# Performance work log

Hardware: AMD Instinct MI355X
Metric: run time of the kernel (lower is better)

Reference implementation:

```python
import jax, jax.numpy as jnp
import numpy as np

B, C, N, K = 4, 192, 8192, 16
C_OUT = 192


def _gather_nodes(xs, idx):
    # xs: [B, C, N], idx: [B, N, K] -> [B, C, N, K]
    return jax.vmap(lambda xb, ib: xb[:, ib])(xs, idx)


def setup_inputs() -> dict:
    key = jax.random.key(0)
    k1, k2, k3 = jax.random.split(key, 3)
    x = jax.random.normal(k1, (B, C, N, 1), dtype=jnp.float32)
    x_0 = jnp.zeros((B, C, N, 1), dtype=jnp.float32)  # unused by forward, kept for interface
    edge_index = jax.random.randint(k2, (2, B, N, K), 0, N, dtype=jnp.int32)
    # 1x1 Conv2d(2C -> C_OUT) weight flattened to [C_OUT, 2C]
    W = jax.random.normal(k3, (C_OUT, 2 * C), dtype=jnp.float32) / np.sqrt(2 * C)
    b = jnp.zeros((C_OUT,), dtype=jnp.float32)
    return {"x": x, "x_0": x_0, "edge_index": edge_index, "W": W, "b": b}


def reference(x, x_0, edge_index, W, b):
    xs = x[..., 0]                       # [B, C, N]
    x_i = _gather_nodes(xs, edge_index[1])   # centers  [B, C, N, K]
    x_j = _gather_nodes(xs, edge_index[0])   # neighbors [B, C, N, K]
    rel = jnp.max(x_j - x_i, axis=-1)        # max-relative [B, C, N]
    y = jnp.concatenate([xs, rel], axis=1)   # [B, 2C, N]
    out = jnp.einsum('oc,bcn->bon', W, y) + b[None, :, None]  # 1x1 conv
    out = jax.nn.relu(out)
    return out[..., None]                # [B, C_OUT, N, 1]
```

## Files before the change

kernel.cpp:

```cpp
#include <hip/hip_runtime.h>
#include <hip/hip_fp16.h>

#define B_    4
#define C_    192
#define N_    8192
#define K_    16
#define O_    192
#define TWOC_ 384
#define BN_   (B_ * N_)
#define NSL_  48

typedef __attribute__((ext_vector_type(8))) _Float16 half8;
typedef __attribute__((ext_vector_type(4))) _Float16 half4v;
typedef __attribute__((ext_vector_type(4))) float floatx4;
typedef __attribute__((ext_vector_type(4))) float fvec4;
typedef __attribute__((ext_vector_type(4))) int   ivec4;
typedef __attribute__((ext_vector_type(4))) unsigned int uvec4;
typedef __attribute__((ext_vector_type(2))) unsigned int uvec2;

__global__ __launch_bounds__(256) void k_prep(const float* __restrict__ x,
                                              const float* __restrict__ W,
                                              unsigned short* __restrict__ xt,
                                              unsigned short* __restrict__ xg,
                                              unsigned short* __restrict__ Wb) {
    int bid = blockIdx.x;
    int tid = threadIdx.x;

    if (bid >= 6144) {
        int base = ((bid - 6144) * 256 + tid) * 16;
        union { unsigned short u[16]; uvec4 v[2]; } o;
#pragma unroll
        for (int q = 0; q < 16; q += 4) {
            fvec4 f = __builtin_nontemporal_load((const fvec4*)(W + base + q));
            union { _Float16 h; unsigned short s; } c;
            c.h = (_Float16)f.x; o.u[q + 0] = c.s;
            c.h = (_Float16)f.y; o.u[q + 1] = c.s;
            c.h = (_Float16)f.z; o.u[q + 2] = c.s;
            c.h = (_Float16)f.w; o.u[q + 3] = c.s;
        }
        *(uvec4*)(Wb + base)     = o.v[0];
        *(uvec4*)(Wb + base + 8) = o.v[1];
        return;
    }

    __shared__ float tile[32][33];
    int xcd  = bid & 7;
    int b    = xcd >> 1;
    int half = xcd & 1;
    int slot = bid >> 3;
    int ct   = slot >> 7;
    int nt   = half * 128 + (slot & 127);
    int c0 = ct * 32, n0 = nt * 32;

    int cc  = tid >> 3;
    int nn4 = (tid & 7) * 4;
    const float* xp = x + ((size_t)b * C_ + c0 + cc) * N_ + n0 + nn4;
    fvec4 v = __builtin_nontemporal_load((const fvec4*)xp);
    tile[nn4 + 0][cc] = v.x;
    tile[nn4 + 1][cc] = v.y;
    tile[nn4 + 2][cc] = v.z;
    tile[nn4 + 3][cc] = v.w;
    __syncthreads();

#pragma unroll
    for (int i = 0; i < 2; i++) {
        int id  = i * 256 + tid;
        int row = id >> 4;
        int ch2 = id & 15;
        union { _Float16 h[2]; unsigned int u; } p;
        p.h[0] = (_Float16)tile[row][ch2 * 2];
        p.h[1] = (_Float16)tile[row][ch2 * 2 + 1];
        *(unsigned int*)(xt + ((size_t)b * N_ + n0 + row) * C_ + c0 + ch2 * 2) = p.u;
    }

    {
        int sl  = tid >> 5;
        int row = tid & 31;
        union { _Float16 h[4]; uvec2 u; } p;
#pragma unroll
        for (int c = 0; c < 4; c++) p.h[c] = (_Float16)tile[row][sl * 4 + c];
        *(uvec2*)(xg + ((size_t)(b * NSL_ + ct * 8 + sl) * N_ + n0 + row) * 4) = p.u;
    }
}

__global__ __launch_bounds__(256) void k_gather(const unsigned short* __restrict__ xg,
                                                const int* __restrict__ eidx,
                                                unsigned short* __restrict__ rt) {
    __shared__ uvec2 lds2[N_];

    int bid = blockIdx.x;
    int xcd = bid & 7;
    int b   = xcd >> 1;
    int nh  = xcd & 1;
    int s   = bid >> 3;
    int tid = threadIdx.x;

    const unsigned short* src = xg + (size_t)(b * NSL_ + s) * N_ * 4;
#pragma unroll
    for (int i = 0; i < 16; i++) {
        int idx = i * 256 + tid;
        uvec4 v = *(const uvec4*)(src + (size_t)idx * 8);
        *(uvec4*)&lds2[idx * 2] = v;
    }
    __syncthreads();

    int nbase = nh * 4096;
    const int* e0 = eidx + (size_t)b * N_ * K_;
    const int* e1 = e0 + (size_t)BN_ * K_;
    unsigned short* rto = rt + (size_t)b * N_ * C_ + s * 4;

#pragma unroll 2
    for (int nn = 0; nn < 16; nn++) {
        int n = nbase + tid * 16 + nn;
        const int* ej = e0 + (size_t)n * K_;
        const int* ei = e1 + (size_t)n * K_;
        ivec4 J[4], I[4];
#pragma unroll
        for (int q = 0; q < 4; q++) {
            J[q] = *(const ivec4*)(ej + q * 4);
            I[q] = *(const ivec4*)(ei + q * 4);
        }
        half4v m;
#pragma unroll
        for (int q = 0; q < 4; q++)
#pragma unroll
            for (int e = 0; e < 4; e++) {
                union { uvec2 u; half4v h; } jv, iv;
                jv.u = lds2[J[q][e]];
                iv.u = lds2[I[q][e]];
                half4v d = jv.h - iv.h;
                m = (q == 0 && e == 0) ? d : __builtin_elementwise_max(m, d);
            }
        union { half4v h; uvec2 u; } o;
        o.h = m;
        *(uvec2*)(rto + (size_t)n * C_) = o.u;
    }
}

__global__ __launch_bounds__(256) void k_conv(const unsigned short* __restrict__ xt,
                                              const unsigned short* __restrict__ rt,
                                              const unsigned short* __restrict__ Wb,
                                              const float* __restrict__ bias,
                                              float* __restrict__ out) {
    __shared__ __align__(16) unsigned short ytile[64 * TWOC_];
    char* yb = (char*)ytile;

    int bid  = blockIdx.x;
    int xcd  = bid & 7;
    int b    = xcd >> 1;
    int slot = bid >> 3;
    int n0   = ((xcd & 1) * 64 + slot) * 64;

    int tid  = threadIdx.x;
    int wave = tid >> 6;
    int lane = tid & 63;
    int m16  = lane & 15;
    int quad = lane >> 4;

    const unsigned short* xsrc = xt + ((size_t)b * N_ + n0) * C_;
    const unsigned short* rsrc = rt + ((size_t)b * N_ + n0) * C_;
#pragma unroll
    for (int i = 0; i < 6; i++) {
        int id = i * 256 + tid;
        int row = id / 24, chunk = id % 24;
        int sw = (row & 7) << 4;
        half8 vx = *(const half8*)(xsrc + (size_t)row * C_ + chunk * 8);
        half8 vr = *(const half8*)(rsrc + (size_t)row * C_ + chunk * 8);
        *(half8*)(yb + row * 768 + ((chunk * 16) ^ sw))       = vx;
        *(half8*)(yb + row * 768 + 384 + ((chunk * 16) ^ sw)) = vr;
    }
    __syncthreads();

    const unsigned short* wbase = Wb + (size_t)(wave * 48 + m16) * TWOC_ + quad * 8;

    floatx4 acc[3][4];
#pragma unroll
    for (int i = 0; i < 3; i++)
#pragma unroll
        for (int j = 0; j < 4; j++) acc[i][j] = (floatx4){0.f, 0.f, 0.f, 0.f};

#pragma unroll 2
    for (int kt = 0; kt < 12; kt++) {
        half8 wf[3], yf[4];
#pragma unroll
        for (int i = 0; i < 3; i++)
            wf[i] = *(const half8*)(wbase + (size_t)(i * 16) * TWOC_ + kt * 32);
#pragma unroll
        for (int j = 0; j < 4; j++) {
            int row = j * 16 + m16;
            yf[j] = *(const half8*)(yb + row * 768 + ((kt * 64 + quad * 16) ^ ((row & 7) << 4)));
        }
#pragma unroll
        for (int i = 0; i < 3; i++)
#pragma unroll
            for (int j = 0; j < 4; j++)
                acc[i][j] = __builtin_amdgcn_mfma_f32_16x16x32_f16(wf[i], yf[j], acc[i][j], 0, 0, 0);
    }

#pragma unroll
    for (int i = 0; i < 3; i++) {
#pragma unroll
        for (int r = 0; r < 4; r++) {
            int o = wave * 48 + i * 16 + quad * 4 + r;
            float bv = bias[o];
#pragma unroll
            for (int j = 0; j < 4; j++) {
                int n = n0 + j * 16 + m16;
                __builtin_nontemporal_store(fmaxf(acc[i][j][r] + bv, 0.f),
                                            &out[((size_t)b * O_ + o) * N_ + n]);
            }
        }
    }
}

extern "C" void kernel_launch(void* const* d_in, const int* in_sizes, int n_in,
                              void* d_out, int out_size, void* d_ws, size_t ws_size,
                              hipStream_t stream) {
    const float* x    = (const float*)d_in[0];
    const int*   eidx = (const int*)d_in[2];
    const float* W    = (const float*)d_in[3];
    const float* bias = (const float*)d_in[4];
    float*       out  = (float*)d_out;

    unsigned short* Wb = (unsigned short*)d_ws;
    unsigned short* xt = (unsigned short*)((char*)d_ws + 147456);
    unsigned short* xg = (unsigned short*)((char*)d_ws + 12730368);
    unsigned short* rt = (unsigned short*)((char*)d_ws + 25313280);

    k_prep<<<dim3(6162), dim3(256), 0, stream>>>(x, W, xt, xg, Wb);
    k_gather<<<dim3(384), dim3(256), 0, stream>>>(xg, eidx, rt);
    k_conv<<<dim3(512), dim3(256), 0, stream>>>(xt, rt, Wb, bias, out);
}
```

Baseline: 157.0 us.

## Drop transposed x copy, store gather output in sliced layout, split gather work

The prep kernel no longer writes a separate node-major fp16 copy of x. The conv kernel now reads both x and the relative-max result from the channel-sliced layout and scatters them into the swizzled LDS tile. The gather kernel writes its output in that same sliced layout with coalesced stores. Its node range is split four ways (four times the blocks), and the next node's edge indices are prefetched in registers. This cuts global write and read traffic and raises gather parallelism, at the cost of reloading the 64KB LDS slice in four times as many blocks and making more, smaller 8-byte LDS writes in conv.

```diff
diff --git a/kernel.cpp b/kernel.cpp
--- a/kernel.cpp
+++ b/kernel.cpp
@@ -20,7 +20,6 @@
 
 __global__ __launch_bounds__(256) void k_prep(const float* __restrict__ x,
                                               const float* __restrict__ W,
-                                              unsigned short* __restrict__ xt,
                                               unsigned short* __restrict__ xg,
                                               unsigned short* __restrict__ Wb) {
     int bid = blockIdx.x;
@@ -62,17 +61,6 @@
     tile[nn4 + 3][cc] = v.w;
     __syncthreads();
 
-#pragma unroll
-    for (int i = 0; i < 2; i++) {
-        int id  = i * 256 + tid;
-        int row = id >> 4;
-        int ch2 = id & 15;
-        union { _Float16 h[2]; unsigned int u; } p;
-        p.h[0] = (_Float16)tile[row][ch2 * 2];
-        p.h[1] = (_Float16)tile[row][ch2 * 2 + 1];
-        *(unsigned int*)(xt + ((size_t)b * N_ + n0 + row) * C_ + c0 + ch2 * 2) = p.u;
-    }
-
     {
         int sl  = tid >> 5;
         int row = tid & 31;
@@ -88,12 +76,29 @@
                                                 unsigned short* __restrict__ rt) {
     __shared__ uvec2 lds2[N_];
 
-    int bid = blockIdx.x;
-    int xcd = bid & 7;
-    int b   = xcd >> 1;
-    int nh  = xcd & 1;
-    int s   = bid >> 3;
-    int tid = threadIdx.x;
+    int bid  = blockIdx.x;
+    int xcd  = bid & 7;
+    int b    = xcd >> 1;
+    int nh   = xcd & 1;
+    int rest = bid >> 3;
+    int s    = rest % NSL_;
+    int sub  = rest / NSL_;
+    int nbase = nh * 4096 + sub * 1024;
+    int tid  = threadIdx.x;
+
+    const int* e0 = eidx + (size_t)b * N_ * K_;
+    const int* e1 = e0 + (size_t)BN_ * K_;
+
+    ivec4 J[4], I[4];
+    {
+        const int* ej = e0 + (size_t)(nbase + tid) * K_;
+        const int* ei = e1 + (size_t)(nbase + tid) * K_;
+#pragma unroll
+        for (int q = 0; q < 4; q++) {
+            J[q] = *(const ivec4*)(ej + q * 4);
+            I[q] = *(const ivec4*)(ei + q * 4);
+        }
+    }
 
     const unsigned short* src = xg + (size_t)(b * NSL_ + s) * N_ * 4;
 #pragma unroll
@@ -104,21 +109,20 @@
     }
     __syncthreads();
 
-    int nbase = nh * 4096;
-    const int* e0 = eidx + (size_t)b * N_ * K_;
-    const int* e1 = e0 + (size_t)BN_ * K_;
-    unsigned short* rto = rt + (size_t)b * N_ * C_ + s * 4;
-
-#pragma unroll 2
-    for (int nn = 0; nn < 16; nn++) {
-        int n = nbase + tid * 16 + nn;
-        const int* ej = e0 + (size_t)n * K_;
-        const int* ei = e1 + (size_t)n * K_;
-        ivec4 J[4], I[4];
-#pragma unroll
-        for (int q = 0; q < 4; q++) {
-            J[q] = *(const ivec4*)(ej + q * 4);
-            I[q] = *(const ivec4*)(ei + q * 4);
+    unsigned short* rto = rt + (size_t)(b * NSL_ + s) * N_ * 4;
+
+#pragma unroll
+    for (int i = 0; i < 4; i++) {
+        int n = nbase + i * 256 + tid;
+        ivec4 Jn[4], In[4];
+        if (i < 3) {
+            const int* ej = e0 + (size_t)(n + 256) * K_;
+            const int* ei = e1 + (size_t)(n + 256) * K_;
+#pragma unroll
+            for (int q = 0; q < 4; q++) {
+                Jn[q] = *(const ivec4*)(ej + q * 4);
+                In[q] = *(const ivec4*)(ei + q * 4);
+            }
         }
         half4v m;
 #pragma unroll
@@ -133,11 +137,13 @@
             }
         union { half4v h; uvec2 u; } o;
         o.h = m;
-        *(uvec2*)(rto + (size_t)n * C_) = o.u;
-    }
-}
-
-__global__ __launch_bounds__(256) void k_conv(const unsigned short* __restrict__ xt,
+        *(uvec2*)(rto + (size_t)n * 4) = o.u;
+#pragma unroll
+        for (int q = 0; q < 4; q++) { J[q] = Jn[q]; I[q] = In[q]; }
+    }
+}
+
+__global__ __launch_bounds__(256) void k_conv(const unsigned short* __restrict__ xg,
                                               const unsigned short* __restrict__ rt,
                                               const unsigned short* __restrict__ Wb,
                                               const float* __restrict__ bias,
@@ -157,17 +163,22 @@
     int m16  = lane & 15;
     int quad = lane >> 4;
 
-    const unsigned short* xsrc = xt + ((size_t)b * N_ + n0) * C_;
-    const unsigned short* rsrc = rt + ((size_t)b * N_ + n0) * C_;
 #pragma unroll
     for (int i = 0; i < 6; i++) {
         int id = i * 256 + tid;
-        int row = id / 24, chunk = id % 24;
-        int sw = (row & 7) << 4;
-        half8 vx = *(const half8*)(xsrc + (size_t)row * C_ + chunk * 8);
-        half8 vr = *(const half8*)(rsrc + (size_t)row * C_ + chunk * 8);
-        *(half8*)(yb + row * 768 + ((chunk * 16) ^ sw))       = vx;
-        *(half8*)(yb + row * 768 + 384 + ((chunk * 16) ^ sw)) = vr;
+        int s  = id >> 5;
+        int np = id & 31;
+        int r1 = np * 2, r2 = np * 2 + 1;
+        size_t goff = ((size_t)(b * NSL_ + s) * N_ + n0 + r1) * 4;
+        uvec4 vx = *(const uvec4*)(xg + goff);
+        uvec4 vr = *(const uvec4*)(rt + goff);
+        uvec2 x1 = {vx.x, vx.y}, x2 = {vx.z, vx.w};
+        uvec2 r1v = {vr.x, vr.y}, r2v = {vr.z, vr.w};
+        int sw1 = (r1 & 7) << 4, sw2 = (r2 & 7) << 4;
+        *(uvec2*)(yb + r1 * 768 + ((s * 8) ^ sw1))         = x1;
+        *(uvec2*)(yb + r2 * 768 + ((s * 8) ^ sw2))         = x2;
+        *(uvec2*)(yb + r1 * 768 + ((384 + s * 8) ^ sw1))   = r1v;
+        *(uvec2*)(yb + r2 * 768 + ((384 + s * 8) ^ sw2))   = r2v;
     }
     __syncthreads();
 
@@ -223,11 +234,10 @@
     float*       out  = (float*)d_out;
 
     unsigned short* Wb = (unsigned short*)d_ws;
-    unsigned short* xt = (unsigned short*)((char*)d_ws + 147456);
-    unsigned short* xg = (unsigned short*)((char*)d_ws + 12730368);
-    unsigned short* rt = (unsigned short*)((char*)d_ws + 25313280);
-
-    k_prep<<<dim3(6162), dim3(256), 0, stream>>>(x, W, xt, xg, Wb);
-    k_gather<<<dim3(384), dim3(256), 0, stream>>>(xg, eidx, rt);
-    k_conv<<<dim3(512), dim3(256), 0, stream>>>(xt, rt, Wb, bias, out);
-}
+    unsigned short* xg = (unsigned short*)((char*)d_ws + 147456);
+    unsigned short* rt = (unsigned short*)((char*)d_ws + 12730368);
+
+    k_prep<<<dim3(6162), dim3(256), 0, stream>>>(x, W, xg, Wb);
+    k_gather<<<dim3(1536), dim3(256), 0, stream>>>(xg, eidx, rt);
+    k_conv<<<dim3(512), dim3(256), 0, stream>>>(xg, rt, Wb, bias, out);
+}
```

New measurement: 134.0 us. -14.6%, faster.
